# Kernel optimization log

Measured on AMD Instinct MI355X. Metric: run time of the kernel, lower is better.

Reference implementation:

```python
import jax, jax.numpy as jnp
import numpy as np

N = 50000
IN, HID, OUT, HEADS = 128, 64, 64, 4


def seg_softmax(logits, seg, num):
    # softmax over edges grouped by destination node; logits [E, H]
    m = jax.ops.segment_max(logits, seg, num_segments=num)
    e = jnp.exp(logits - m[seg])
    s = jax.ops.segment_sum(e, seg, num_segments=num)
    return e / (s[seg] + 1e-16)


def gat_conv(x, src, dst, W, a_s, a_d, b, heads, concat):
    n = x.shape[0]
    h = (x @ W.T).reshape(n, heads, -1)           # [N, H, C]
    alpha_src = jnp.einsum('nhc,hc->nh', h, a_s)   # per-node src score
    alpha_dst = jnp.einsum('nhc,hc->nh', h, a_d)
    logits = jax.nn.leaky_relu(alpha_src[src] + alpha_dst[dst], 0.2)  # [E, H]
    alpha = seg_softmax(logits, dst, n)
    out = jax.ops.segment_sum(alpha[:, :, None] * h[src], dst, num_segments=n)  # [N, H, C]
    out = out.reshape(n, -1) if concat else out.mean(axis=1)
    return out + b


def setup_inputs():
    key = jax.random.key(0)
    ks = jax.random.split(key, 16)
    x = jax.random.normal(ks[0], (N, IN), dtype=jnp.float32)
    edge_index = jax.random.randint(ks[1], (2, 800000), 0, N, dtype=jnp.int64)

    def glorot(k, shape):
        fan = shape[-1]
        return jax.random.normal(k, shape, dtype=jnp.float32) / jnp.sqrt(jnp.float32(fan))

    d = {"x": x, "edge_index": edge_index}
    # layer 1: IN -> HID, HEADS heads, concat
    d["W1"] = glorot(ks[2], (HEADS * HID, IN))
    d["as1"] = glorot(ks[3], (HEADS, HID))
    d["ad1"] = glorot(ks[4], (HEADS, HID))
    d["b1"] = jnp.zeros((HEADS * HID,), jnp.float32)
    # layer 2: HID*HEADS -> HID, HEADS heads, concat
    d["W2"] = glorot(ks[5], (HEADS * HID, HEADS * HID))
    d["as2"] = glorot(ks[6], (HEADS, HID))
    d["ad2"] = glorot(ks[7], (HEADS, HID))
    d["b2"] = jnp.zeros((HEADS * HID,), jnp.float32)
    # layer 3: HID*HEADS -> OUT, 1 head
    d["W3"] = glorot(ks[8], (OUT, HEADS * HID))
    d["as3"] = glorot(ks[9], (1, OUT))
    d["ad3"] = glorot(ks[10], (1, OUT))
    d["b3"] = jnp.zeros((OUT,), jnp.float32)
    return d


def reference(x, edge_index, W1, as1, ad1, b1, W2, as2, ad2, b2, W3, as3, ad3, b3):
    # PyG GATConv adds self-loops by default
    loops = jnp.arange(N, dtype=edge_index.dtype)
    src = jnp.concatenate([edge_index[0], loops])
    dst = jnp.concatenate([edge_index[1], loops])

    h = jax.nn.relu(gat_conv(x, src, dst, W1, as1, ad1, b1, HEADS, True))
    h = jax.nn.relu(gat_conv(h, src, dst, W2, as2, ad2, b2, HEADS, True))
    out = gat_conv(h, src, dst, W3, as3, ad3, b3, 1, True)
    return out
```

## Files before the change

### kernel.cpp

```cpp
#include <hip/hip_runtime.h>
#include <hip/hip_bf16.h>
#include <math.h>


typedef __bf16 bf16x8 __attribute__((ext_vector_type(8)));
typedef float f32x4 __attribute__((ext_vector_type(4)));
typedef _Float16 half8v __attribute__((ext_vector_type(8)));
typedef _Float16 half4v __attribute__((ext_vector_type(4)));

#define MPAD 50048
#define QINV 2048.0f
#define QDQ  4.8828125e-4f

__device__ __forceinline__ void gload_lds16(const void* g, void* l) {
  __builtin_amdgcn_global_load_lds(
      (const __attribute__((address_space(1))) unsigned int*)g,
      (__attribute__((address_space(3))) unsigned int*)l, 16, 0, 0);
}

__device__ __forceinline__ unsigned int splitf(float a) {
  __hip_bfloat16 h = __float2bfloat16(a);
  float hf = __bfloat162float(h);
  __hip_bfloat16 l = __float2bfloat16(a - hf);
  return (unsigned int)__builtin_bit_cast(unsigned short, h) |
         ((unsigned int)__builtin_bit_cast(unsigned short, l) << 16);
}

__device__ __forceinline__ float leaky02(float l) {
  return (l >= 0.f) ? l : 0.2f * l;
}

__device__ __forceinline__ short quant16(float v) {
  int q = (int)rintf(v * QINV);
  q = q > 32767 ? 32767 : (q < -32768 ? -32768 : q);
  return (short)q;
}


__global__ void init_counts_kernel(int* counts, int n) {
  int i = blockIdx.x * blockDim.x + threadIdx.x;
  if (i < n) counts[i] = 1;
}

__global__ void hist_kernel(const int* __restrict__ dst, int e, int* counts) {
  int i = blockIdx.x * blockDim.x + threadIdx.x;
  if (i < e) atomicAdd(&counts[dst[i]], 1);
}

__global__ __launch_bounds__(1024) void block_sum_kernel(const int* __restrict__ counts,
                                                         int* __restrict__ bsum, int n) {
  __shared__ int red[1024];
  int i = blockIdx.x * 1024 + threadIdx.x;
  red[threadIdx.x] = (i < n) ? counts[i] : 0;
  __syncthreads();
  #pragma unroll
  for (int off = 512; off > 0; off >>= 1) {
    if (threadIdx.x < off) red[threadIdx.x] += red[threadIdx.x + off];
    __syncthreads();
  }
  if (threadIdx.x == 0) bsum[blockIdx.x] = red[0];
}

__global__ void scan_sums_kernel(int* bsum, int nb) {
  int t = threadIdx.x;
  int c = (t < nb) ? bsum[t] : 0;
  int v = c;
  #pragma unroll
  for (int off = 1; off < 64; off <<= 1) {
    int u = __shfl_up(v, off);
    if (t >= off) v += u;
  }
  if (t < nb) bsum[t] = v - c;
}

__global__ __launch_bounds__(1024) void scan_final_kernel(const int* __restrict__ counts,
    const int* __restrict__ bsum, int* __restrict__ offsets, int* __restrict__ cursor, int n) {
  __shared__ int sc[1024];
  int i = blockIdx.x * 1024 + threadIdx.x;
  int c = (i < n) ? counts[i] : 0;
  sc[threadIdx.x] = c;
  __syncthreads();
  for (int off = 1; off < 1024; off <<= 1) {
    int v = 0;
    if (threadIdx.x >= off) v = sc[threadIdx.x - off];
    __syncthreads();
    sc[threadIdx.x] += v;
    __syncthreads();
  }
  int excl = sc[threadIdx.x] - c + bsum[blockIdx.x];
  if (i < n) {
    offsets[i] = excl;
    cursor[i] = excl;
  } else if (i == n) {
    offsets[n] = excl;
  }
}

__global__ void scatter_kernel(const int* __restrict__ src, const int* __restrict__ dst,
                               int e800, int etot, int* cursor, int* __restrict__ ssrc) {
  int i = blockIdx.x * blockDim.x + threadIdx.x;
  if (i >= etot) return;
  int s, d;
  if (i < e800) { s = src[i]; d = dst[i]; }
  else          { s = i - e800; d = s; }
  int pos = atomicAdd(&cursor[d], 1);
  ssrc[pos] = s;
}


__global__ void cvtx_kernel(const float* __restrict__ in, _Float16* __restrict__ out, int count4) {
  int i = blockIdx.x * blockDim.x + threadIdx.x;
  if (i >= count4) return;
  float4 v = reinterpret_cast<const float4*>(in)[i];
  half4v h = {(_Float16)v.x, (_Float16)v.y, (_Float16)v.z, (_Float16)v.w};
  *reinterpret_cast<half4v*>(out + (size_t)i * 4) = h;
}

__global__ void cvtW_kernel(const float* __restrict__ W1, const float* __restrict__ W2,
                            const float* __restrict__ W3, _Float16* __restrict__ o1,
                            _Float16* __restrict__ o2, uint4* __restrict__ o3) {
  int i = blockIdx.x * blockDim.x + threadIdx.x;
  if (i < 8192) {
    float4 v = reinterpret_cast<const float4*>(W1)[i];
    half4v h = {(_Float16)v.x, (_Float16)v.y, (_Float16)v.z, (_Float16)v.w};
    *reinterpret_cast<half4v*>(o1 + (size_t)i * 4) = h;
  } else if (i < 8192 + 16384) {
    int j = i - 8192;
    float4 v = reinterpret_cast<const float4*>(W2)[j];
    half4v h = {(_Float16)v.x, (_Float16)v.y, (_Float16)v.z, (_Float16)v.w};
    *reinterpret_cast<half4v*>(o2 + (size_t)j * 4) = h;
  } else if (i < 8192 + 16384 + 4096) {
    int j = i - (8192 + 16384);
    float4 v = reinterpret_cast<const float4*>(W3)[j];
    uint4 o;
    o.x = splitf(v.x); o.y = splitf(v.y); o.z = splitf(v.z); o.w = splitf(v.w);
    o3[j] = o;
  }
}

template <int KP, int BM, int BN, int WAVES_M, int WAVES_N, int OTOT, int HEADS,
          bool F16IN, bool F16OUT>
__global__ __launch_bounds__(256) void gemm2_kernel(
    const unsigned short* __restrict__ A, const unsigned short* __restrict__ B,
    void* __restrict__ Cq, const float* __restrict__ a_s, const float* __restrict__ a_d,
    float* __restrict__ asrcO, float* __restrict__ adstO, int M) {
  constexpr int BK = 64;
  constexpr int NK = KP / BK;
  constexpr int MFRAG = BM / WAVES_M / 16;
  constexpr int NFRAG = BN / WAVES_N / 16;
  __shared__ unsigned short As[2][BM * BK];
  __shared__ unsigned short Bs[2][BN * BK];

  const int tid = threadIdx.x;
  const int lane = tid & 63;
  const int wid = tid >> 6;
  const int m0 = blockIdx.x * BM;
  const int o0 = blockIdx.y * BN;

  const int srow = tid >> 3;
  const int scolb = (tid & 7) * 16;
  const int sswz = (srow & 7) << 4;
  const char* aSrc = (const char*)A + (size_t)(m0 + srow) * (KP * 2) + (scolb ^ sswz);
  const char* bSrc = (const char*)B + (size_t)(o0 + srow) * (KP * 2) + (scolb ^ sswz);
  char* aDst0 = (char*)&As[0][0] + wid * 1024;
  char* bDst0 = (char*)&Bs[0][0] + wid * 1024;

  auto stage = [&](int buf, int kt) {
    const size_t ko = (size_t)kt * 128;
    char* ad = aDst0 + buf * (BM * 128);
    #pragma unroll
    for (int i = 0; i < BM / 32; ++i)
      gload_lds16(aSrc + ko + (size_t)i * 32 * (KP * 2), ad + i * 4096);
    char* bd = bDst0 + buf * (BN * 128);
    #pragma unroll
    for (int j = 0; j < BN / 32; ++j)
      gload_lds16(bSrc + ko + (size_t)j * 32 * (KP * 2), bd + j * 4096);
  };

  const int fr = lane & 15;
  const int fg = lane >> 4;
  const int fswz = (fr & 7) << 4;
  const int wm0 = (wid / WAVES_N) * (BM / WAVES_M);
  const int wn0 = (wid % WAVES_N) * (BN / WAVES_N);

  f32x4 acc[MFRAG][NFRAG];
  #pragma unroll
  for (int mi = 0; mi < MFRAG; ++mi)
    #pragma unroll
    for (int ni = 0; ni < NFRAG; ++ni) acc[mi][ni] = (f32x4)0.f;

  stage(0, 0);
  __syncthreads();

  for (int kt = 0; kt < NK; ++kt) {
    const int buf = kt & 1;
    if (kt + 1 < NK) stage(buf ^ 1, kt + 1);
    const char* asB = (const char*)&As[buf][0] + (wm0 + fr) * 128;
    const char* bsB = (const char*)&Bs[buf][0] + (wn0 + fr) * 128;
    #pragma unroll
    for (int kh = 0; kh < 2; ++kh) {
      const int kb = (kh * 64 + fg * 16) ^ fswz;
      if constexpr (F16IN) {
        half8v af[MFRAG], bfr[NFRAG];
        #pragma unroll
        for (int mi = 0; mi < MFRAG; ++mi)
          af[mi] = *reinterpret_cast<const half8v*>(asB + mi * 16 * 128 + kb);
        #pragma unroll
        for (int ni = 0; ni < NFRAG; ++ni)
          bfr[ni] = *reinterpret_cast<const half8v*>(bsB + ni * 16 * 128 + kb);
        #pragma unroll
        for (int mi = 0; mi < MFRAG; ++mi)
          #pragma unroll
          for (int ni = 0; ni < NFRAG; ++ni)
            acc[mi][ni] = __builtin_amdgcn_mfma_f32_16x16x32_f16(af[mi], bfr[ni], acc[mi][ni], 0, 0, 0);
      } else {
        bf16x8 af[MFRAG], bfr[NFRAG];
        #pragma unroll
        for (int mi = 0; mi < MFRAG; ++mi)
          af[mi] = *reinterpret_cast<const bf16x8*>(asB + mi * 16 * 128 + kb);
        #pragma unroll
        for (int ni = 0; ni < NFRAG; ++ni)
          bfr[ni] = *reinterpret_cast<const bf16x8*>(bsB + ni * 16 * 128 + kb);
        #pragma unroll
        for (int mi = 0; mi < MFRAG; ++mi)
          #pragma unroll
          for (int ni = 0; ni < NFRAG; ++ni)
            acc[mi][ni] = __builtin_amdgcn_mfma_f32_16x16x32_bf16(af[mi], bfr[ni], acc[mi][ni], 0, 0, 0);
      }
    }
    __syncthreads();
  }

  const int head = (HEADS == 4) ? ((o0 + wn0) >> 6) : 0;
  float asl[NFRAG], adl[NFRAG];
  #pragma unroll
  for (int ni = 0; ni < NFRAG; ++ni) {
    int c64 = (HEADS == 4) ? (ni * 16 + fr) : (wn0 + ni * 16 + fr);
    asl[ni] = a_s[head * 64 + c64];
    adl[ni] = a_d[head * 64 + c64];
  }
  #pragma unroll
  for (int mi = 0; mi < MFRAG; ++mi) {
    #pragma unroll
    for (int r = 0; r < 4; ++r) {
      int row = m0 + wm0 + mi * 16 + fg * 4 + r;
      float ps = 0.f, pd = 0.f;
      #pragma unroll
      for (int ni = 0; ni < NFRAG; ++ni) {
        ps = fmaf(acc[mi][ni][r], asl[ni], ps);
        pd = fmaf(acc[mi][ni][r], adl[ni], pd);
      }
      #pragma unroll
      for (int off = 1; off < 16; off <<= 1) {
        ps += __shfl_xor(ps, off);
        pd += __shfl_xor(pd, off);
      }
      if (row < M) {
        if (fr == 0) {
          asrcO[(size_t)row * HEADS + head] = ps;
          adstO[(size_t)row * HEADS + head] = pd;
        }
        #pragma unroll
        for (int ni = 0; ni < NFRAG; ++ni) {
          size_t ci = (size_t)row * OTOT + o0 + wn0 + ni * 16 + fr;
          if constexpr (F16OUT) ((_Float16*)Cq)[ci] = (_Float16)acc[mi][ni][r];
          else                  ((short*)Cq)[ci] = quant16(acc[mi][ni][r]);
        }
      }
    }
  }
}

template <bool OUTBF>
__global__ __launch_bounds__(256) void aggregate4_kernel(
    const _Float16* __restrict__ hq, const float* __restrict__ asrc,
    const float* __restrict__ adst, const float* __restrict__ bias,
    const int* __restrict__ offsets, const int* __restrict__ ssrc,
    void* __restrict__ outp, int n) {
  int wid = threadIdx.x >> 6;
  int lane = threadIdx.x & 63;
  int sub = lane >> 5;
  int hl = lane & 31;
  int node = blockIdx.x * 8 + wid * 2 + sub;
  if (node >= n) return;
  int head = hl >> 3;
  int ch8 = hl * 8;
  float adv = adst[(size_t)node * 4 + head];
  int beg = offsets[node], end = offsets[node + 1];

  float s0 = 0.f, s1 = 0.f, s2 = 0.f, s3 = 0.f;
  float A0[8] = {}, A1[8] = {}, A2[8] = {}, A3[8] = {};
  int e = beg;
  for (; e + 3 < end; e += 4) {
    int c0 = ssrc[e + 0], c1 = ssrc[e + 1], c2 = ssrc[e + 2], c3 = ssrc[e + 3];
    float p0 = __expf(leaky02(asrc[(size_t)c0 * 4 + head] + adv));
    float p1 = __expf(leaky02(asrc[(size_t)c1 * 4 + head] + adv));
    float p2 = __expf(leaky02(asrc[(size_t)c2 * 4 + head] + adv));
    float p3 = __expf(leaky02(asrc[(size_t)c3 * 4 + head] + adv));
    half8v h0 = *reinterpret_cast<const half8v*>(&hq[(size_t)c0 * 256 + ch8]);
    half8v h1 = *reinterpret_cast<const half8v*>(&hq[(size_t)c1 * 256 + ch8]);
    half8v h2 = *reinterpret_cast<const half8v*>(&hq[(size_t)c2 * 256 + ch8]);
    half8v h3 = *reinterpret_cast<const half8v*>(&hq[(size_t)c3 * 256 + ch8]);
    s0 += p0; s1 += p1; s2 += p2; s3 += p3;
    #pragma unroll
    for (int j = 0; j < 8; ++j) {
      A0[j] = fmaf((float)h0[j], p0, A0[j]);
      A1[j] = fmaf((float)h1[j], p1, A1[j]);
      A2[j] = fmaf((float)h2[j], p2, A2[j]);
      A3[j] = fmaf((float)h3[j], p3, A3[j]);
    }
  }
  for (; e < end; ++e) {
    int c0 = ssrc[e];
    float p0 = __expf(leaky02(asrc[(size_t)c0 * 4 + head] + adv));
    half8v h0 = *reinterpret_cast<const half8v*>(&hq[(size_t)c0 * 256 + ch8]);
    s0 += p0;
    #pragma unroll
    for (int j = 0; j < 8; ++j) A0[j] = fmaf((float)h0[j], p0, A0[j]);
  }
  float s = (s0 + s1) + (s2 + s3);
  float A[8];
  #pragma unroll
  for (int j = 0; j < 8; ++j) A[j] = (A0[j] + A1[j]) + (A2[j] + A3[j]);

  float inv = 1.f / (s + 1e-16f);
  float4 bv0 = *reinterpret_cast<const float4*>(&bias[ch8]);
  float4 bv1 = *reinterpret_cast<const float4*>(&bias[ch8 + 4]);
  float o[8];
  o[0] = fmaxf(A[0] * inv + bv0.x, 0.f);
  o[1] = fmaxf(A[1] * inv + bv0.y, 0.f);
  o[2] = fmaxf(A[2] * inv + bv0.z, 0.f);
  o[3] = fmaxf(A[3] * inv + bv0.w, 0.f);
  o[4] = fmaxf(A[4] * inv + bv1.x, 0.f);
  o[5] = fmaxf(A[5] * inv + bv1.y, 0.f);
  o[6] = fmaxf(A[6] * inv + bv1.z, 0.f);
  o[7] = fmaxf(A[7] * inv + bv1.w, 0.f);
  if (OUTBF) {
    uint4 pk0, pk1;
    pk0.x = splitf(o[0]); pk0.y = splitf(o[1]); pk0.z = splitf(o[2]); pk0.w = splitf(o[3]);
    pk1.x = splitf(o[4]); pk1.y = splitf(o[5]); pk1.z = splitf(o[6]); pk1.w = splitf(o[7]);
    reinterpret_cast<uint4*>(outp)[(size_t)node * 64 + hl * 2 + 0] = pk0;
    reinterpret_cast<uint4*>(outp)[(size_t)node * 64 + hl * 2 + 1] = pk1;
  } else {
    half8v hv;
    #pragma unroll
    for (int j = 0; j < 8; ++j) hv[j] = (_Float16)o[j];
    *reinterpret_cast<half8v*>((_Float16*)outp + (size_t)node * 256 + ch8) = hv;
  }
}

__global__ __launch_bounds__(256) void aggregate1_kernel(
    const short* __restrict__ hq, const float* __restrict__ asrc,
    const float* __restrict__ adst, const float* __restrict__ bias,
    const int* __restrict__ offsets, const int* __restrict__ ssrc,
    float* __restrict__ out, int n) {
  int wid = threadIdx.x >> 6;
  int lane = threadIdx.x & 63;
  int node = blockIdx.x * 4 + wid;
  if (node >= n) return;
  int g = lane >> 4;
  int w = lane & 15;
  float adv = adst[node];
  int beg = offsets[node], end = offsets[node + 1];

  float s = 0.f;
  float4 A = {0, 0, 0, 0};
  int e0 = beg;
  for (; e0 + 3 < end; e0 += 4) {
    int src = ssrc[e0 + g];
    float p = __expf(leaky02(asrc[src] + adv));
    short4 q = *reinterpret_cast<const short4*>(&hq[(size_t)src * 64 + w * 4]);
    s += p;
    A.x += p * (float)q.x; A.y += p * (float)q.y;
    A.z += p * (float)q.z; A.w += p * (float)q.w;
  }
  if (e0 + g < end) {
    int src = ssrc[e0 + g];
    float p = __expf(leaky02(asrc[src] + adv));
    short4 q = *reinterpret_cast<const short4*>(&hq[(size_t)src * 64 + w * 4]);
    s += p;
    A.x += p * (float)q.x; A.y += p * (float)q.y;
    A.z += p * (float)q.z; A.w += p * (float)q.w;
  }
  #pragma unroll
  for (int off = 16; off < 64; off <<= 1) {
    s += __shfl_xor(s, off);
    A.x += __shfl_xor(A.x, off);
    A.y += __shfl_xor(A.y, off);
    A.z += __shfl_xor(A.z, off);
    A.w += __shfl_xor(A.w, off);
  }
  if (g == 0) {
    float inv = QDQ / (s + 1e-16f);
    float4 bv = *reinterpret_cast<const float4*>(&bias[w * 4]);
    float4 o;
    o.x = A.x * inv + bv.x;
    o.y = A.y * inv + bv.y;
    o.z = A.z * inv + bv.z;
    o.w = A.w * inv + bv.w;
    *reinterpret_cast<float4*>(&out[(size_t)node * 64 + w * 4]) = o;
  }
}


extern "C" void kernel_launch(void* const* d_in, const int* in_sizes, int n_in,
                              void* d_out, int out_size, void* d_ws, size_t ws_size,
                              hipStream_t stream) {
  const float* x   = (const float*)d_in[0];
  const int*   ei  = (const int*)d_in[1];
  const float* W1  = (const float*)d_in[2];
  const float* as1 = (const float*)d_in[3];
  const float* ad1 = (const float*)d_in[4];
  const float* b1  = (const float*)d_in[5];
  const float* W2  = (const float*)d_in[6];
  const float* as2 = (const float*)d_in[7];
  const float* ad2 = (const float*)d_in[8];
  const float* b2  = (const float*)d_in[9];
  const float* W3  = (const float*)d_in[10];
  const float* as3 = (const float*)d_in[11];
  const float* ad3 = (const float*)d_in[12];
  const float* b3  = (const float*)d_in[13];
  float* out = (float*)d_out;

  const int n    = in_sizes[0] / 128;
  const int e800 = in_sizes[1] / 2;
  const int etot = e800 + n;

  char* ws = (char*)d_ws;
  size_t off = 0;
  auto alloc = [&](size_t bytes) -> void* {
    void* p = ws + off;
    off = (off + bytes + 255) & ~(size_t)255;
    return p;
  };
  _Float16*       x16      = (_Float16*)alloc((size_t)MPAD * 128 * 2);
  _Float16*       feat16   = (_Float16*)alloc((size_t)MPAD * 256 * 2);
  _Float16*       hagg16   = (_Float16*)alloc((size_t)MPAD * 256 * 2);
  unsigned short* hsplitBF = (unsigned short*)alloc((size_t)MPAD * 512 * 2);
  short*          featL3   = (short*)alloc((size_t)MPAD * 64 * 2);
  _Float16*       w1f      = (_Float16*)alloc((size_t)256 * 128 * 2);
  _Float16*       w2f      = (_Float16*)alloc((size_t)256 * 256 * 2);
  unsigned short* w3s      = (unsigned short*)alloc((size_t)64 * 512 * 2);
  float* asrc    = (float*)alloc((size_t)n * 4 * 4);
  float* adst    = (float*)alloc((size_t)n * 4 * 4);
  int*   ssrc    = (int*)alloc((size_t)(etot + 4) * 4);
  int*   offsets = (int*)alloc((size_t)(n + 1) * 4);
  int*   cursor  = (int*)alloc((size_t)n * 4);
  int*   counts  = (int*)alloc((size_t)n * 4);
  int*   bsum    = (int*)alloc((size_t)64 * 4);

  const int* esrc = ei;
  const int* edst = ei + e800;
  const int nbScan = (n + 1024) / 1024;

  init_counts_kernel<<<(n + 255) / 256, 256, 0, stream>>>(counts, n);
  hist_kernel<<<(e800 + 255) / 256, 256, 0, stream>>>(edst, e800, counts);
  block_sum_kernel<<<nbScan, 1024, 0, stream>>>(counts, bsum, n);
  scan_sums_kernel<<<1, 64, 0, stream>>>(bsum, nbScan);
  scan_final_kernel<<<nbScan, 1024, 0, stream>>>(counts, bsum, offsets, cursor, n);
  scatter_kernel<<<(etot + 255) / 256, 256, 0, stream>>>(esrc, edst, e800, etot, cursor, ssrc);

  cvtx_kernel<<<(n * 128 / 4 + 255) / 256, 256, 0, stream>>>(x, x16, n * 128 / 4);
  cvtW_kernel<<<(8192 + 16384 + 4096 + 255) / 256, 256, 0, stream>>>(
      W1, W2, W3, w1f, w2f, (uint4*)w3s);

  const int mBlocks = MPAD / 128;

  gemm2_kernel<128, 128, 128, 2, 2, 256, 4, true, true><<<dim3(mBlocks, 2), 256, 0, stream>>>(
      (const unsigned short*)x16, (const unsigned short*)w1f, feat16, as1, ad1, asrc, adst, n);
  aggregate4_kernel<false><<<(n + 7) / 8, 256, 0, stream>>>(
      feat16, asrc, adst, b1, offsets, ssrc, hagg16, n);

  gemm2_kernel<256, 128, 128, 2, 2, 256, 4, true, true><<<dim3(mBlocks, 2), 256, 0, stream>>>(
      (const unsigned short*)hagg16, (const unsigned short*)w2f, feat16, as2, ad2, asrc, adst, n);
  aggregate4_kernel<true><<<(n + 7) / 8, 256, 0, stream>>>(
      feat16, asrc, adst, b2, offsets, ssrc, hsplitBF, n);

  gemm2_kernel<512, 128, 64, 4, 1, 64, 1, false, false><<<dim3(mBlocks, 1), 256, 0, stream>>>(
      hsplitBF, w3s, featL3, as3, ad3, asrc, adst, n);
  aggregate1_kernel<<<(n + 3) / 4, 256, 0, stream>>>(
      featL3, asrc, adst, b3, offsets, ssrc, out, n);
}
```

Measured before the change: 335.2 us.

## Sort per-node source lists and merge conversion kernels, memset counts

Adds a wave-level bitonic sort of each destination node's source indices (degrees 3 to 64) after the CSR scatter, so the later gathers of feature rows in the aggregation kernels touch memory in ascending address order and get better cache locality. It also replaces the init-to-one kernel with a memset plus a +1 added inside the scan kernels, and merges the x and weight conversion kernels into one launch. The sort adds an extra pass over the edge list and changes the summation order within each segment.

```diff
diff --git a/kernel.cpp b/kernel.cpp
--- a/kernel.cpp
+++ b/kernel.cpp
@@ -37,11 +37,6 @@
 }
 
 
-__global__ void init_counts_kernel(int* counts, int n) {
-  int i = blockIdx.x * blockDim.x + threadIdx.x;
-  if (i < n) counts[i] = 1;
-}
-
 __global__ void hist_kernel(const int* __restrict__ dst, int e, int* counts) {
   int i = blockIdx.x * blockDim.x + threadIdx.x;
   if (i < e) atomicAdd(&counts[dst[i]], 1);
@@ -51,7 +46,7 @@
                                                          int* __restrict__ bsum, int n) {
   __shared__ int red[1024];
   int i = blockIdx.x * 1024 + threadIdx.x;
-  red[threadIdx.x] = (i < n) ? counts[i] : 0;
+  red[threadIdx.x] = (i < n) ? (counts[i] + 1) : 0;
   __syncthreads();
   #pragma unroll
   for (int off = 512; off > 0; off >>= 1) {
@@ -77,7 +72,7 @@
     const int* __restrict__ bsum, int* __restrict__ offsets, int* __restrict__ cursor, int n) {
   __shared__ int sc[1024];
   int i = blockIdx.x * 1024 + threadIdx.x;
-  int c = (i < n) ? counts[i] : 0;
+  int c = (i < n) ? (counts[i] + 1) : 0;
   sc[threadIdx.x] = c;
   __syncthreads();
   for (int off = 1; off < 1024; off <<= 1) {
@@ -107,34 +102,57 @@
   ssrc[pos] = s;
 }
 
-
-__global__ void cvtx_kernel(const float* __restrict__ in, _Float16* __restrict__ out, int count4) {
+__global__ __launch_bounds__(256) void sortseg_kernel(const int* __restrict__ offsets,
+                                                      int* __restrict__ ssrc, int n) {
+  int wid = threadIdx.x >> 6;
+  int lane = threadIdx.x & 63;
+  int node = blockIdx.x * 4 + wid;
+  if (node >= n) return;
+  int beg = offsets[node], end = offsets[node + 1];
+  int deg = end - beg;
+  if (deg > 64 || deg < 3) return;
+  int v = (lane < deg) ? ssrc[beg + lane] : 0x7fffffff;
+  #pragma unroll
+  for (int k = 2; k <= 64; k <<= 1) {
+    #pragma unroll
+    for (int j = k >> 1; j > 0; j >>= 1) {
+      int other = __shfl_xor(v, j);
+      bool up = ((lane & k) == 0);
+      bool lower = ((lane & j) == 0);
+      int mn = min(v, other), mx = max(v, other);
+      v = (lower == up) ? mn : mx;
+    }
+  }
+  if (lane < deg) ssrc[beg + lane] = v;
+}
+
+__global__ void cvt_all_kernel(const float* __restrict__ x, const float* __restrict__ W1,
+                               const float* __restrict__ W2, const float* __restrict__ W3,
+                               _Float16* __restrict__ x16, _Float16* __restrict__ o1,
+                               _Float16* __restrict__ o2, uint4* __restrict__ o3, int nx4) {
   int i = blockIdx.x * blockDim.x + threadIdx.x;
-  if (i >= count4) return;
-  float4 v = reinterpret_cast<const float4*>(in)[i];
-  half4v h = {(_Float16)v.x, (_Float16)v.y, (_Float16)v.z, (_Float16)v.w};
-  *reinterpret_cast<half4v*>(out + (size_t)i * 4) = h;
-}
-
-__global__ void cvtW_kernel(const float* __restrict__ W1, const float* __restrict__ W2,
-                            const float* __restrict__ W3, _Float16* __restrict__ o1,
-                            _Float16* __restrict__ o2, uint4* __restrict__ o3) {
-  int i = blockIdx.x * blockDim.x + threadIdx.x;
-  if (i < 8192) {
-    float4 v = reinterpret_cast<const float4*>(W1)[i];
+  if (i < nx4) {
+    float4 v = reinterpret_cast<const float4*>(x)[i];
     half4v h = {(_Float16)v.x, (_Float16)v.y, (_Float16)v.z, (_Float16)v.w};
-    *reinterpret_cast<half4v*>(o1 + (size_t)i * 4) = h;
-  } else if (i < 8192 + 16384) {
-    int j = i - 8192;
-    float4 v = reinterpret_cast<const float4*>(W2)[j];
+    *reinterpret_cast<half4v*>(x16 + (size_t)i * 4) = h;
+    return;
+  }
+  int j = i - nx4;
+  if (j < 8192) {
+    float4 v = reinterpret_cast<const float4*>(W1)[j];
     half4v h = {(_Float16)v.x, (_Float16)v.y, (_Float16)v.z, (_Float16)v.w};
-    *reinterpret_cast<half4v*>(o2 + (size_t)j * 4) = h;
-  } else if (i < 8192 + 16384 + 4096) {
-    int j = i - (8192 + 16384);
-    float4 v = reinterpret_cast<const float4*>(W3)[j];
+    *reinterpret_cast<half4v*>(o1 + (size_t)j * 4) = h;
+  } else if (j < 8192 + 16384) {
+    int k = j - 8192;
+    float4 v = reinterpret_cast<const float4*>(W2)[k];
+    half4v h = {(_Float16)v.x, (_Float16)v.y, (_Float16)v.z, (_Float16)v.w};
+    *reinterpret_cast<half4v*>(o2 + (size_t)k * 4) = h;
+  } else if (j < 8192 + 16384 + 4096) {
+    int k = j - (8192 + 16384);
+    float4 v = reinterpret_cast<const float4*>(W3)[k];
     uint4 o;
     o.x = splitf(v.x); o.y = splitf(v.y); o.z = splitf(v.z); o.w = splitf(v.w);
-    o3[j] = o;
+    o3[k] = o;
   }
 }
 
@@ -453,16 +471,17 @@
   const int* edst = ei + e800;
   const int nbScan = (n + 1024) / 1024;
 
-  init_counts_kernel<<<(n + 255) / 256, 256, 0, stream>>>(counts, n);
+  hipMemsetAsync(counts, 0, (size_t)n * 4, stream);
   hist_kernel<<<(e800 + 255) / 256, 256, 0, stream>>>(edst, e800, counts);
   block_sum_kernel<<<nbScan, 1024, 0, stream>>>(counts, bsum, n);
   scan_sums_kernel<<<1, 64, 0, stream>>>(bsum, nbScan);
   scan_final_kernel<<<nbScan, 1024, 0, stream>>>(counts, bsum, offsets, cursor, n);
   scatter_kernel<<<(etot + 255) / 256, 256, 0, stream>>>(esrc, edst, e800, etot, cursor, ssrc);
-
-  cvtx_kernel<<<(n * 128 / 4 + 255) / 256, 256, 0, stream>>>(x, x16, n * 128 / 4);
-  cvtW_kernel<<<(8192 + 16384 + 4096 + 255) / 256, 256, 0, stream>>>(
-      W1, W2, W3, w1f, w2f, (uint4*)w3s);
+  sortseg_kernel<<<(n + 3) / 4, 256, 0, stream>>>(offsets, ssrc, n);
+
+  const int nx4 = n * 128 / 4;
+  cvt_all_kernel<<<(nx4 + 28672 + 255) / 256, 256, 0, stream>>>(
+      x, W1, W2, W3, x16, w1f, w2f, (uint4*)w3s, nx4);
 
   const int mBlocks = MPAD / 128;
 
```

New measurement: 346.3 us. +3.3%, slower.
